# Kernel tuning notes

Hardware: AMD Instinct MI355X
Metric: run time of the kernel (lower is better)

Reference implementation:

```python
import jax, jax.numpy as jnp
import numpy as np

EPS = 1e-5

def _bn(x, g, b):
    # training-mode BatchNorm1d: per-feature batch stats (biased var), affine
    mu = jnp.mean(x, 0)
    var = jnp.var(x, 0)
    return (x - mu) * jax.lax.rsqrt(var + EPS) * g + b

def _sage(x_src, x_dst, src, dst, Wl, bl, Wr):
    # PyG SAGEConv(mean): lin_l(mean_{j in N(i)} x_j) + lin_r(x_i); lin_r has no bias
    n = x_dst.shape[0]
    s = jax.ops.segment_sum(x_src[src], dst, num_segments=n)          # [N_dst, H]
    c = jax.ops.segment_sum(jnp.ones(src.shape, x_src.dtype), dst, num_segments=n)
    m = s / jnp.maximum(c, 1.0)[:, None]                              # mean aggregation; isolated nodes -> 0
    return m @ Wl + bl + x_dst @ Wr


def setup_inputs() -> dict:
    ND, NG, NS = 30000, 60000, 15000
    FD, FG, FS = 256, 128, 64
    H, O = 128, 64
    E = dict(dg=500000, gd=500000, gs=400000, sg=400000, ds=150000, sd=150000)
    keys = iter(jax.random.split(jax.random.key(0), 64))
    def nrm(shape, s=0.05):
        return jax.random.normal(next(keys), shape, jnp.float32) * s
    def ridx(n, hi):
        return jax.random.randint(next(keys), (n,), 0, hi, jnp.int32)
    inp = {
        'x_drug': nrm((ND, FD), 1.0), 'x_gene': nrm((NG, FG), 1.0), 'x_dis': nrm((NS, FS), 1.0),
        'src_dg': ridx(E['dg'], ND), 'dst_dg': ridx(E['dg'], NG),
        'src_gd': ridx(E['gd'], NG), 'dst_gd': ridx(E['gd'], ND),
        'src_gs': ridx(E['gs'], NG), 'dst_gs': ridx(E['gs'], NS),
        'src_sg': ridx(E['sg'], NS), 'dst_sg': ridx(E['sg'], NG),
        'src_ds': ridx(E['ds'], ND), 'dst_ds': ridx(E['ds'], NS),
        'src_sd': ridx(E['sd'], NS), 'dst_sd': ridx(E['sd'], ND),
        # input projections per node type
        'W_in_drug': nrm((FD, H)), 'b_in_drug': jnp.zeros((H,), jnp.float32),
        'W_in_gene': nrm((FG, H)), 'b_in_gene': jnp.zeros((H,), jnp.float32),
        'W_in_dis':  nrm((FS, H)), 'b_in_dis':  jnp.zeros((H,), jnp.float32),
        # input norms, [3 node types, H]
        'g_in': jnp.ones((3, H), jnp.float32), 'bt_in': jnp.zeros((3, H), jnp.float32),
        # SAGEConv weights: [3 layers, 6 edge types, H, H]; order: dg,gd,gs,sg,ds,sd
        'Wl': nrm((3, 6, H, H)), 'Wr': nrm((3, 6, H, H)), 'bl': jnp.zeros((3, 6, H), jnp.float32),
        # per-layer per-type norms [3 layers, 3 types, H]
        'g_conv': jnp.ones((3, 3, H), jnp.float32), 'bt_conv': jnp.zeros((3, 3, H), jnp.float32),
        'W_fin': nrm((H, O)), 'b_fin': jnp.zeros((O,), jnp.float32),
    }
    return inp


def reference(x_drug, x_gene, x_dis,
              src_dg, dst_dg, src_gd, dst_gd, src_gs, dst_gs,
              src_sg, dst_sg, src_ds, dst_ds, src_sd, dst_sd,
              W_in_drug, b_in_drug, W_in_gene, b_in_gene, W_in_dis, b_in_dis,
              g_in, bt_in, Wl, Wr, bl, g_conv, bt_conv, W_fin, b_fin):
    relu = jax.nn.relu
    # input proj + BN + ReLU (dropout in eval mode = identity)
    hd = relu(_bn(x_drug @ W_in_drug + b_in_drug, g_in[0], bt_in[0]))
    hg = relu(_bn(x_gene @ W_in_gene + b_in_gene, g_in[1], bt_in[1]))
    hs = relu(_bn(x_dis  @ W_in_dis  + b_in_dis,  g_in[2], bt_in[2]))
    for L in range(3):
        rd, rg, rs = hd, hg, hs
        # HeteroConv aggr='mean' over the two edge types hitting each dst type
        od = ( _sage(rg, rd, src_gd, dst_gd, Wl[L,1], bl[L,1], Wr[L,1])
             + _sage(rs, rd, src_sd, dst_sd, Wl[L,5], bl[L,5], Wr[L,5]) ) * 0.5
        og = ( _sage(rd, rg, src_dg, dst_dg, Wl[L,0], bl[L,0], Wr[L,0])
             + _sage(rs, rg, src_sg, dst_sg, Wl[L,3], bl[L,3], Wr[L,3]) ) * 0.5
        os_ = ( _sage(rg, rs, src_gs, dst_gs, Wl[L,2], bl[L,2], Wr[L,2])
              + _sage(rd, rs, src_ds, dst_ds, Wl[L,4], bl[L,4], Wr[L,4]) ) * 0.5
        hd = relu(_bn(od,  g_conv[L,0], bt_conv[L,0])) + rd
        hg = relu(_bn(og,  g_conv[L,1], bt_conv[L,1])) + rg
        hs = relu(_bn(os_, g_conv[L,2], bt_conv[L,2])) + rs
    return (hd @ W_fin + b_fin, hg @ W_fin + b_fin, hs @ W_fin + b_fin)
```

## Files before the change

### kernel.cpp

```cpp
#include <hip/hip_runtime.h>
#include <cstddef>
#include <cstdint>

typedef _Float16 f16;
typedef _Float16 f16x8 __attribute__((ext_vector_type(8)));
typedef float f32x4 __attribute__((ext_vector_type(4)));

constexpr int ND = 30000, NG = 60000, NS = 15000;
constexpr float BN_EPS = 1e-5f;
constexpr int NBUCK = 64;
constexpr int TBUCK = 6 * NBUCK;
constexpr int PCHUNK = 4096;

static inline int cdiv(int a, int b){ return (a + b - 1) / b; }


struct BDesc {
    const int* src[6]; const int* dst[6];
    int Ebase[7]; int shift[6]; int N[6];
    int* bCnt; int* bBase; int* bCursor;
    uint2* packed;
    int* offs[6]; int* csr[6];
};

__global__ __launch_bounds__(256) void bhist_k(BDesc bd){
    __shared__ int hist[TBUCK];
    int tid = threadIdx.x;
    for (int i = tid; i < TBUCK; i += 256) hist[i] = 0;
    __syncthreads();
    int Etot = bd.Ebase[6];
    #pragma unroll
    for (int u = 0; u < 16; u++){
        int e = blockIdx.x * PCHUNK + u * 256 + tid;
        if (e < Etot){
            int t = 0;
            #pragma unroll
            for (int i = 1; i < 6; i++) if (e >= bd.Ebase[i]) t = i;
            int d = bd.dst[t][e - bd.Ebase[t]];
            atomicAdd(&hist[t * NBUCK + (d >> bd.shift[t])], 1);
        }
    }
    __syncthreads();
    for (int i = tid; i < TBUCK; i += 256)
        if (hist[i]) atomicAdd(&bd.bCnt[i], hist[i]);
}

__global__ __launch_bounds__(512) void bscan_k(BDesc bd){
    __shared__ int sh[TBUCK];
    int tid = threadIdx.x;
    int my = (tid < TBUCK) ? bd.bCnt[tid] : 0;
    if (tid < TBUCK) sh[tid] = my;
    __syncthreads();
    for (int d = 1; d < TBUCK; d <<= 1){
        int v = (tid < TBUCK) ? sh[tid] : 0;
        int add = (tid >= d && tid < TBUCK) ? sh[tid - d] : 0;
        __syncthreads();
        if (tid < TBUCK) sh[tid] = v + add;
        __syncthreads();
    }
    if (tid < TBUCK){
        int excl = sh[tid] - my;
        bd.bBase[tid] = excl;
        bd.bCursor[tid] = excl;
    }
    if (tid == 0) bd.bBase[TBUCK] = sh[TBUCK - 1];
}

__global__ __launch_bounds__(256) void bpart_k(BDesc bd){
    __shared__ int hist[TBUCK];
    __shared__ int basesh[TBUCK];
    int tid = threadIdx.x;
    for (int i = tid; i < TBUCK; i += 256) hist[i] = 0;
    __syncthreads();
    int Etot = bd.Ebase[6];
    int mb[16], mr[16], ms[16], md[16];
    #pragma unroll
    for (int u = 0; u < 16; u++){
        int e = blockIdx.x * PCHUNK + u * 256 + tid;
        mb[u] = -1;
        if (e < Etot){
            int t = 0;
            #pragma unroll
            for (int i = 1; i < 6; i++) if (e >= bd.Ebase[i]) t = i;
            int le = e - bd.Ebase[t];
            int s = bd.src[t][le], d = bd.dst[t][le];
            int b = t * NBUCK + (d >> bd.shift[t]);
            mr[u] = atomicAdd(&hist[b], 1);
            mb[u] = b; ms[u] = s; md[u] = d;
        }
    }
    __syncthreads();
    for (int i = tid; i < TBUCK; i += 256)
        basesh[i] = hist[i] ? atomicAdd(&bd.bCursor[i], hist[i]) : 0;
    __syncthreads();
    #pragma unroll
    for (int u = 0; u < 16; u++){
        if (mb[u] >= 0){
            int pos = basesh[mb[u]] + mr[u];
            bd.packed[pos] = make_uint2((unsigned)ms[u], (unsigned)md[u]);
        }
    }
}

__global__ __launch_bounds__(256) void bucketCsr_k(BDesc bd){
    __shared__ int cnt[1024];
    __shared__ int sh[256];
    int b = blockIdx.x;
    int t = b >> 6;
    int bb = b & 63;
    int tid = threadIdx.x;
    int shift = bd.shift[t];
    int nodeBase = bb << shift;
    int Nt = bd.N[t];
    int span = 1 << shift;
    int tbase = bd.bBase[t * NBUCK];
    int eBeg = bd.bBase[b], eEnd = bd.bBase[b + 1];
    int bLocal = eBeg - tbase;
    #pragma unroll
    for (int i = 0; i < 4; i++) cnt[tid + i * 256] = 0;
    __syncthreads();
    for (int e = eBeg + tid; e < eEnd; e += 256)
        atomicAdd(&cnt[(int)bd.packed[e].y - nodeBase], 1);
    __syncthreads();
    int c0 = cnt[tid * 4], c1 = cnt[tid * 4 + 1], c2 = cnt[tid * 4 + 2], c3 = cnt[tid * 4 + 3];
    int s = c0 + c1 + c2 + c3;
    sh[tid] = s;
    __syncthreads();
    for (int d = 1; d < 256; d <<= 1){
        int v = sh[tid];
        int add = (tid >= d) ? sh[tid - d] : 0;
        __syncthreads();
        sh[tid] = v + add;
        __syncthreads();
    }
    int run = sh[tid] - s;
    int idx = tid * 4;
    int ex0 = run, ex1 = run + c0, ex2 = ex1 + c1, ex3 = ex2 + c2;
    if (idx     < span && nodeBase + idx     < Nt) bd.offs[t][nodeBase + idx]     = bLocal + ex0;
    if (idx + 1 < span && nodeBase + idx + 1 < Nt) bd.offs[t][nodeBase + idx + 1] = bLocal + ex1;
    if (idx + 2 < span && nodeBase + idx + 2 < Nt) bd.offs[t][nodeBase + idx + 2] = bLocal + ex2;
    if (idx + 3 < span && nodeBase + idx + 3 < Nt) bd.offs[t][nodeBase + idx + 3] = bLocal + ex3;
    cnt[idx] = ex0; cnt[idx + 1] = ex1; cnt[idx + 2] = ex2; cnt[idx + 3] = ex3;
    __syncthreads();
    for (int e = eBeg + tid; e < eEnd; e += 256){
        uint2 p = bd.packed[e];
        int lpos = atomicAdd(&cnt[(int)p.y - nodeBase], 1);
        bd.csr[t][bLocal + lpos] = (int)p.x;
    }
    if (bb == NBUCK - 1 && tid == 0)
        bd.offs[t][Nt] = bd.bBase[(t + 1) * NBUCK] - tbase;
}


struct CastDesc { const float* src[3]; f16* dst[3]; int base[4]; };

__global__ __launch_bounds__(256) void castAll_k(CastDesc cdsc){
    int idx = blockIdx.x * 256 + threadIdx.x;
    if (idx >= cdsc.base[3]) return;
    int t = 0;
    #pragma unroll
    for (int i = 1; i < 3; i++) if (idx >= cdsc.base[i]) t = i;
    int i4 = (idx - cdsc.base[t]) * 4;
    float4 v = *reinterpret_cast<const float4*>(cdsc.src[t] + i4);
    union { uint2 u; f16 h[4]; } o;
    o.h[0] = (f16)v.x; o.h[1] = (f16)v.y; o.h[2] = (f16)v.z; o.h[3] = (f16)v.w;
    *reinterpret_cast<uint2*>(cdsc.dst[t] + i4) = o.u;
}

struct WDesc {
    const float* W_in0; const float* W_in1; const float* W_in2;
    const float* W_fin; const float* Wl; const float* Wr;
    f16* Wint0; f16* Wint1; f16* Wint2; f16* Wfin_t; f16* Wcat_t;
};

__global__ __launch_bounds__(256) void weightAll_k(WDesc wd){
    int idx = blockIdx.x * 256 + threadIdx.x;
    if (idx < 32768){
        int c = idx >> 8, k = idx & 255;
        wd.Wint0[idx] = (f16)wd.W_in0[k * 128 + c];
    } else if (idx < 49152){
        int l = idx - 32768; int c = l >> 7, k = l & 127;
        wd.Wint1[l] = (f16)wd.W_in1[k * 128 + c];
    } else if (idx < 57344){
        int l = idx - 49152; int c = l >> 6, k = l & 63;
        wd.Wint2[l] = (f16)wd.W_in2[k * 128 + c];
    } else if (idx < 65536){
        int l = idx - 57344; int c = l >> 7, k = l & 127;
        wd.Wfin_t[l] = (f16)wd.W_fin[k * 64 + c];
    } else if (idx < 507904){
        int l = idx - 65536;
        int g = l / (384 * 128);
        int rem = l - g * (384 * 128);
        int c = rem / 384;
        int k = rem - c * 384;
        int L = g / 3, t = g - L * 3;
        const int e1s[3] = {1, 0, 2}, e2s[3] = {5, 3, 4};
        int e1 = e1s[t], e2 = e2s[t];
        float v;
        if (k < 128)      v = wd.Wl[(((size_t)L * 6 + e1) * 128 + k) * 128 + c];
        else if (k < 256) v = wd.Wl[(((size_t)L * 6 + e2) * 128 + (k - 128)) * 128 + c];
        else {
            int kr = k - 256;
            v = wd.Wr[(((size_t)L * 6 + e1) * 128 + kr) * 128 + c]
              + wd.Wr[(((size_t)L * 6 + e2) * 128 + kr) * 128 + c];
        }
        wd.Wcat_t[l] = (f16)v;
    }
}


struct GSeg { const int* offs; const int* csr; const uint4* h; uint4* A; int colPair4; int N; int base; };
struct GDesc { GSeg s[6]; const uint4* zrow; };

__device__ __forceinline__ f16x8 as_h8(uint4 v){
    union { uint4 u; f16x8 h; } c; c.u = v; return c.h;
}

__device__ __forceinline__ f16x8 shfl_xor8(f16x8 v, int mask){
    union { f16x8 h; int u[4]; } c; c.h = v;
    #pragma unroll
    for (int i = 0; i < 4; i++) c.u[i] = __shfl_xor(c.u[i], mask);
    return c.h;
}

__global__ __launch_bounds__(256) void gatherall_k(GDesc gd){
    int bid = blockIdx.x;
    int si = 0;
    #pragma unroll
    for (int t = 1; t < 6; t++) if (bid >= gd.s[t].base) si = t;
    GSeg sg = gd.s[si];
    int node = (bid - sg.base) * 4 + (threadIdx.x >> 6);
    if (node >= sg.N) return;
    int lane = threadIdx.x & 63;
    int grp = lane >> 4, li = lane & 15;
    int s = sg.offs[node], e = sg.offs[node + 1];
    const int* cp = sg.csr;
    const uint4* hp = sg.h;
    f16x8 a = {};
    for (int c = s; c < e; c += 64){
        int nchunk = e - c; if (nchunk > 64) nchunk = 64;
        int idx = (lane < nchunk) ? cp[c + lane] : 0;
        int r = 0;
        for (; r + 32 <= nchunk; r += 32){
            int i0 = __shfl(idx, r + grp);
            int i1 = __shfl(idx, r + 4  + grp);
            int i2 = __shfl(idx, r + 8  + grp);
            int i3 = __shfl(idx, r + 12 + grp);
            int i4 = __shfl(idx, r + 16 + grp);
            int i5 = __shfl(idx, r + 20 + grp);
            int i6 = __shfl(idx, r + 24 + grp);
            int i7 = __shfl(idx, r + 28 + grp);
            uint4 v0 = hp[(size_t)i0 * 16 + li];
            uint4 v1 = hp[(size_t)i1 * 16 + li];
            uint4 v2 = hp[(size_t)i2 * 16 + li];
            uint4 v3 = hp[(size_t)i3 * 16 + li];
            uint4 v4 = hp[(size_t)i4 * 16 + li];
            uint4 v5 = hp[(size_t)i5 * 16 + li];
            uint4 v6 = hp[(size_t)i6 * 16 + li];
            uint4 v7 = hp[(size_t)i7 * 16 + li];
            a = a + as_h8(v0); a = a + as_h8(v1); a = a + as_h8(v2); a = a + as_h8(v3);
            a = a + as_h8(v4); a = a + as_h8(v5); a = a + as_h8(v6); a = a + as_h8(v7);
        }
        if (r + 16 <= nchunk){
            int i0 = __shfl(idx, r + grp);
            int i1 = __shfl(idx, r + 4  + grp);
            int i2 = __shfl(idx, r + 8  + grp);
            int i3 = __shfl(idx, r + 12 + grp);
            uint4 v0 = hp[(size_t)i0 * 16 + li];
            uint4 v1 = hp[(size_t)i1 * 16 + li];
            uint4 v2 = hp[(size_t)i2 * 16 + li];
            uint4 v3 = hp[(size_t)i3 * 16 + li];
            a = a + as_h8(v0); a = a + as_h8(v1); a = a + as_h8(v2); a = a + as_h8(v3);
            r += 16;
        }
        for (; r < nchunk; r += 4){
            int ei = __shfl(idx, r + grp);
            const uint4* rp = ((r + grp) < nchunk) ? (hp + (size_t)ei * 16) : gd.zrow;
            a = a + as_h8(rp[li]);
        }
    }
    a = a + shfl_xor8(a, 16);
    a = a + shfl_xor8(a, 32);
    if (grp == 0){
        float inv = (e > s) ? 1.0f / (float)(e - s) : 0.f;
        union { uint4 u; f16 h[8]; } pk;
        #pragma unroll
        for (int i = 0; i < 8; i++) pk.h[i] = (f16)((float)a[i] * inv);
        sg.A[(size_t)node * 32 + sg.colPair4 + li] = pk.u;
    }
}


struct GemmSeg {
    const f16* A1; const f16* A2; const f16* Wt;
    const float* b1; const float* b2; void* out; float* stats;
    int lda1, lda2, ksplit, N, K, tileBase; float scale;
};
struct GemmDesc { GemmSeg s[3]; };

template<int BN, bool STATS, bool OUT16>
__global__ __launch_bounds__(256) void gemmAll_k(GemmDesc gd){
    constexpr int CF = BN / 16;
    __shared__ f16 As[128 * 64];
    __shared__ f16 Bs[BN * 64];
    __shared__ float ssum[BN];
    __shared__ float ssq[BN];
    int bid = blockIdx.x;
    int si = 0;
    #pragma unroll
    for (int t = 1; t < 3; t++) if (bid >= gd.s[t].tileBase) si = t;
    GemmSeg sg = gd.s[si];
    int tid = threadIdx.x;
    int wv = tid >> 6, lane = tid & 63;
    int row0 = (bid - sg.tileBase) * 128;
    int N = sg.N, K = sg.K;
    if (STATS && tid < BN){ ssum[tid] = 0.f; ssq[tid] = 0.f; }

    int rsub = lane >> 3;
    int seg  = lane & 7;
    int sseg = seg ^ rsub;

    f32x4 acc[2][CF];
    #pragma unroll
    for (int rf = 0; rf < 2; rf++)
        #pragma unroll
        for (int cf = 0; cf < CF; cf++)
            acc[rf][cf] = (f32x4){0.f, 0.f, 0.f, 0.f};

    for (int k0 = 0; k0 < K; k0 += 64){
        const f16* Ab; int lda, kloc;
        if (k0 < sg.ksplit){ Ab = sg.A1; lda = sg.lda1; kloc = k0; }
        else               { Ab = sg.A2; lda = sg.lda2; kloc = k0 - sg.ksplit; }
        #pragma unroll
        for (int p = 0; p < 4; p++){
            int r = wv * 32 + p * 8 + rsub;
            const f16* srca = Ab + (size_t)(row0 + r) * lda + kloc + sseg * 8;
            __builtin_amdgcn_global_load_lds(
                (const __attribute__((address_space(1))) void*)srca,
                (__attribute__((address_space(3))) void*)&As[(wv * 32 + p * 8) * 64],
                16, 0, 0);
        }
        #pragma unroll
        for (int p = 0; p < BN / 32; p++){
            int c0 = wv * (BN / 4) + p * 8;
            const f16* srcb = sg.Wt + (size_t)(c0 + rsub) * K + k0 + sseg * 8;
            __builtin_amdgcn_global_load_lds(
                (const __attribute__((address_space(1))) void*)srcb,
                (__attribute__((address_space(3))) void*)&Bs[c0 * 64],
                16, 0, 0);
        }
        __syncthreads();
        #pragma unroll
        for (int kf = 0; kf < 2; kf++){
            int kidx = kf * 4 + (lane >> 4);
            int ar0 = wv * 32 + (lane & 15);
            int ar1 = ar0 + 16;
            f16x8 a0 = *reinterpret_cast<const f16x8*>(&As[ar0 * 64 + ((kidx ^ (ar0 & 7)) * 8)]);
            f16x8 a1 = *reinterpret_cast<const f16x8*>(&As[ar1 * 64 + ((kidx ^ (ar1 & 7)) * 8)]);
            #pragma unroll
            for (int cf = 0; cf < CF; cf++){
                int bc = cf * 16 + (lane & 15);
                f16x8 b = *reinterpret_cast<const f16x8*>(&Bs[bc * 64 + ((kidx ^ (bc & 7)) * 8)]);
                acc[0][cf] = __builtin_amdgcn_mfma_f32_16x16x32_f16(a0, b, acc[0][cf], 0, 0, 0);
                acc[1][cf] = __builtin_amdgcn_mfma_f32_16x16x32_f16(a1, b, acc[1][cf], 0, 0, 0);
            }
        }
        __syncthreads();
    }
    int rbase = row0 + wv * 32 + ((lane >> 4) << 2);
    #pragma unroll
    for (int cf = 0; cf < CF; cf++){
        int col = cf * 16 + (lane & 15);
        float bias = 0.f;
        if (sg.b1) bias += sg.b1[col];
        if (sg.b2) bias += sg.b2[col];
        float ls = 0.f, lq = 0.f;
        #pragma unroll
        for (int rf = 0; rf < 2; rf++){
            #pragma unroll
            for (int q = 0; q < 4; q++){
                int gr = rbase + rf * 16 + q;
                if (gr < N){
                    float v = sg.scale * (acc[rf][cf][q] + bias);
                    if (OUT16) ((f16*)sg.out)[(size_t)gr * BN + col] = (f16)v;
                    else       ((float*)sg.out)[(size_t)gr * BN + col] = v;
                    ls += v; lq += v * v;
                }
            }
        }
        if (STATS){ atomicAdd(&ssum[col], ls); atomicAdd(&ssq[col], lq); }
    }
    if (STATS){
        __syncthreads();
        if (tid < BN){
            atomicAdd(&sg.stats[tid], ssum[tid]);
            atomicAdd(&sg.stats[128 + tid], ssq[tid]);
        }
    }
}


struct BnSeg { const f16* o; const float* stats; const float* g; const float* b; f16* h; int N; float invN; int residual; int idxBase; };
struct BnDesc { BnSeg s[3]; int total; };

__global__ __launch_bounds__(256) void bnAll_k(BnDesc bd){
    int idx = blockIdx.x * 256 + threadIdx.x;
    if (idx >= bd.total) return;
    int si = 0;
    #pragma unroll
    for (int t = 1; t < 3; t++) if (idx >= bd.s[t].idxBase) si = t;
    BnSeg sg = bd.s[si];
    int l = idx - sg.idxBase;
    int n = l >> 4, c8 = (l & 15) * 8;
    union { uint4 u; f16 h[8]; } ov;
    ov.u = *reinterpret_cast<const uint4*>(sg.o + (size_t)n * 128 + c8);
    float r[8];
    #pragma unroll
    for (int j = 0; j < 8; j++){
        int c = c8 + j;
        float mu  = sg.stats[c] * sg.invN;
        float var = sg.stats[128 + c] * sg.invN - mu * mu;
        float v = ((float)ov.h[j] - mu) * rsqrtf(var + BN_EPS) * sg.g[c] + sg.b[c];
        r[j] = v > 0.f ? v : 0.f;
    }
    f16* hp = sg.h + (size_t)n * 128 + c8;
    if (sg.residual){
        uint4 old = *reinterpret_cast<const uint4*>(hp);
        union { uint4 u; f16 h[8]; } ou; ou.u = old;
        #pragma unroll
        for (int j = 0; j < 8; j++) r[j] += (float)ou.h[j];
    }
    union { uint4 u; f16 h[8]; } pk;
    #pragma unroll
    for (int j = 0; j < 8; j++) pk.h[j] = (f16)r[j];
    *reinterpret_cast<uint4*>(hp) = pk.u;
}


extern "C" void kernel_launch(void* const* d_in, const int* in_sizes, int n_in,
                              void* d_out, int out_size, void* d_ws, size_t ws_size,
                              hipStream_t stream){
    const float* x_drug = (const float*)d_in[0];
    const float* x_gene = (const float*)d_in[1];
    const float* x_dis  = (const float*)d_in[2];
    const int* srcP[6] = {(const int*)d_in[3], (const int*)d_in[5], (const int*)d_in[7],
                          (const int*)d_in[9], (const int*)d_in[11], (const int*)d_in[13]};
    const int* dstP[6] = {(const int*)d_in[4], (const int*)d_in[6], (const int*)d_in[8],
                          (const int*)d_in[10], (const int*)d_in[12], (const int*)d_in[14]};
    const int  Et[6]   = {in_sizes[3], in_sizes[5], in_sizes[7], in_sizes[9], in_sizes[11], in_sizes[13]};
    const float* W_in[3] = {(const float*)d_in[15], (const float*)d_in[17], (const float*)d_in[19]};
    const float* b_in[3] = {(const float*)d_in[16], (const float*)d_in[18], (const float*)d_in[20]};
    const float* g_in  = (const float*)d_in[21];
    const float* bt_in = (const float*)d_in[22];
    const float* Wl    = (const float*)d_in[23];
    const float* Wr    = (const float*)d_in[24];
    const float* bl    = (const float*)d_in[25];
    const float* g_conv  = (const float*)d_in[26];
    const float* bt_conv = (const float*)d_in[27];
    const float* W_fin = (const float*)d_in[28];
    const float* b_fin = (const float*)d_in[29];
    float* out = (float*)d_out;

    const int Ndst_t[6]     = {NG, ND, NS, NG, NS, ND};
    const int srcT[6]       = {0, 1, 1, 2, 0, 2};
    const int dstT[6]       = {1, 0, 2, 1, 2, 0};
    const int colPair4_t[6] = {0, 0, 0, 16, 16, 16};

    const int Nn[3]  = {ND, NG, NS};
    const int Kin[3] = {256, 128, 64};
    const float* xin[3] = {x_drug, x_gene, x_dis};

    char* base = (char*)d_ws;
    size_t off = 0;
    auto alloc = [&](size_t bytes) -> char* {
        char* p = base + off; off += (bytes + 255) & ~(size_t)255; return p;
    };
    f16* h[3];  for (int t = 0; t < 3; t++) h[t]  = (f16*)alloc((size_t)Nn[t] * 128 * 2);
    f16* A[3];  for (int t = 0; t < 3; t++) A[t]  = (f16*)alloc((size_t)Nn[t] * 256 * 2);
    f16* xb[3]; for (int t = 0; t < 3; t++) xb[t] = (f16*)alloc((size_t)Nn[t] * Kin[t] * 2);
    f16* Wint[3]; for (int t = 0; t < 3; t++) Wint[t] = (f16*)alloc((size_t)128 * Kin[t] * 2);
    f16* Wfin_t = (f16*)alloc((size_t)64 * 128 * 2);
    f16* Wcat_t = (f16*)alloc((size_t)9 * 128 * 384 * 2);
    char* oPool = alloc((size_t)(ND + NG + NS) * 128 * 2);
    f16* o[3];
    o[0] = (f16*)oPool; o[1] = o[0] + (size_t)ND * 128; o[2] = o[1] + (size_t)NG * 128;
    uint2* packed = (uint2*)oPool;
    float* stats = (float*)alloc(12 * 256 * 4);
    int* zeroPool = (int*)alloc((size_t)(TBUCK + 64) * 4);
    int* bCnt = zeroPool;
    const uint4* zrow = (const uint4*)(zeroPool + TBUCK);
    int* bBase   = (int*)alloc((TBUCK + 1) * 4);
    int* bCursor = (int*)alloc(TBUCK * 4);
    int *offs[6], *csr[6];
    for (int t = 0; t < 6; t++) offs[t] = (int*)alloc((size_t)(Ndst_t[t] + 1) * 4);
    for (int t = 0; t < 6; t++) csr[t]  = (int*)alloc((size_t)Et[t] * 4);

    hipMemsetAsync(zeroPool, 0, (size_t)(TBUCK + 64) * 4, stream);
    hipMemsetAsync(stats, 0, 12 * 256 * 4, stream);

    BDesc bd;
    {
        int ecum = 0;
        for (int t = 0; t < 6; t++){
            bd.src[t] = srcP[t]; bd.dst[t] = dstP[t];
            bd.Ebase[t] = ecum; ecum += Et[t];
            int sft = 0; while (((Ndst_t[t] - 1) >> sft) >= NBUCK) sft++;
            bd.shift[t] = sft;
            bd.N[t] = Ndst_t[t];
            bd.offs[t] = offs[t]; bd.csr[t] = csr[t];
        }
        bd.Ebase[6] = ecum;
        bd.bCnt = bCnt; bd.bBase = bBase; bd.bCursor = bCursor;
        bd.packed = packed;
    }
    int Etot = bd.Ebase[6];
    bhist_k<<<cdiv(Etot, PCHUNK), 256, 0, stream>>>(bd);
    bscan_k<<<1, 512, 0, stream>>>(bd);
    bpart_k<<<cdiv(Etot, PCHUNK), 256, 0, stream>>>(bd);
    bucketCsr_k<<<TBUCK, 256, 0, stream>>>(bd);

    CastDesc cds;
    {
        int b = 0;
        for (int t = 0; t < 3; t++){
            cds.src[t] = xin[t]; cds.dst[t] = xb[t];
            cds.base[t] = b; b += Nn[t] * Kin[t] / 4;
        }
        cds.base[3] = b;
    }
    castAll_k<<<cdiv(cds.base[3], 256), 256, 0, stream>>>(cds);
    WDesc wd = {W_in[0], W_in[1], W_in[2], W_fin, Wl, Wr,
                Wint[0], Wint[1], Wint[2], Wfin_t, Wcat_t};
    weightAll_k<<<cdiv(507904, 256), 256, 0, stream>>>(wd);

    int tiles[3]; for (int t = 0; t < 3; t++) tiles[t] = cdiv(Nn[t], 128);
    int tileBase[4] = {0, tiles[0], tiles[0] + tiles[1], tiles[0] + tiles[1] + tiles[2]};

    {
        GemmDesc g{};
        for (int t = 0; t < 3; t++){
            g.s[t] = {xb[t], xb[t], Wint[t], b_in[t], nullptr, o[t], stats + t * 256,
                      Kin[t], Kin[t], Kin[t], Nn[t], Kin[t], tileBase[t], 1.0f};
        }
        gemmAll_k<128, true, true><<<tileBase[3], 256, 0, stream>>>(g);
        BnDesc bnd{}; int ib = 0;
        for (int t = 0; t < 3; t++){
            bnd.s[t] = {o[t], stats + t * 256, g_in + t * 128, bt_in + t * 128, h[t],
                        Nn[t], 1.0f / Nn[t], 0, ib};
            ib += Nn[t] * 16;
        }
        bnd.total = ib;
        bnAll_k<<<cdiv(ib, 256), 256, 0, stream>>>(bnd);
    }

    const int e1s[3] = {1, 0, 2}, e2s[3] = {5, 3, 4};
    for (int L = 0; L < 3; L++){
        GDesc gd; int bacc = 0;
        gd.zrow = zrow;
        for (int t = 0; t < 6; t++){
            gd.s[t].offs = offs[t];
            gd.s[t].csr  = csr[t];
            gd.s[t].h    = (const uint4*)h[srcT[t]];
            gd.s[t].A    = (uint4*)A[dstT[t]];
            gd.s[t].colPair4 = colPair4_t[t];
            gd.s[t].N    = Ndst_t[t];
            gd.s[t].base = bacc;
            bacc += cdiv(Ndst_t[t], 4);
        }
        gatherall_k<<<bacc, 256, 0, stream>>>(gd);
        GemmDesc g{};
        for (int t = 0; t < 3; t++){
            int e1 = e1s[t], e2 = e2s[t];
            g.s[t] = {A[t], h[t], Wcat_t + (size_t)(L * 3 + t) * 128 * 384,
                      bl + (size_t)(L * 6 + e1) * 128, bl + (size_t)(L * 6 + e2) * 128,
                      o[t], stats + (size_t)(3 + L * 3 + t) * 256,
                      256, 128, 256, Nn[t], 384, tileBase[t], 0.5f};
        }
        gemmAll_k<128, true, true><<<tileBase[3], 256, 0, stream>>>(g);
        BnDesc bnd{}; int ib = 0;
        for (int t = 0; t < 3; t++){
            bnd.s[t] = {o[t], stats + (size_t)(3 + L * 3 + t) * 256,
                        g_conv + (size_t)(L * 3 + t) * 128, bt_conv + (size_t)(L * 3 + t) * 128,
                        h[t], Nn[t], 1.0f / Nn[t], 1, ib};
            ib += Nn[t] * 16;
        }
        bnd.total = ib;
        bnAll_k<<<cdiv(ib, 256), 256, 0, stream>>>(bnd);
    }

    {
        int Ntot = ND + NG + NS;
        GemmDesc g{};
        g.s[0] = {h[0], h[0], Wfin_t, b_fin, nullptr, out, nullptr,
                  128, 128, 128, Ntot, 128, 0, 1.0f};
        g.s[1] = g.s[0]; g.s[1].tileBase = 0x3FFFFFFF; g.s[1].N = 0;
        g.s[2] = g.s[1];
        gemmAll_k<64, false, false><<<cdiv(Ntot, 128), 256, 0, stream>>>(g);
    }
}
```

Measured before the change: 612.3 us.

## Map one 16-lane group per destination node in the neighbor gather kernel

The gather kernel now gives each destination node a 16-lane group instead of a full 64-lane wavefront, so 16 nodes share a block. Each group walks the node's neighbor list 8 at a time, loading indices directly rather than broadcasting them through shuffles. This removes the cross-lane reduction and the idle lanes on low-degree nodes (average degree about 5 to 30). The trade-off is less memory-level parallelism per node for high-degree nodes, redundant index loads across the 16 lanes, and extra loads from the zero row at the end of each list.

```diff
diff --git a/kernel.cpp b/kernel.cpp
--- a/kernel.cpp
+++ b/kernel.cpp
@@ -216,78 +216,39 @@
     union { uint4 u; f16x8 h; } c; c.u = v; return c.h;
 }
 
-__device__ __forceinline__ f16x8 shfl_xor8(f16x8 v, int mask){
-    union { f16x8 h; int u[4]; } c; c.h = v;
-    #pragma unroll
-    for (int i = 0; i < 4; i++) c.u[i] = __shfl_xor(c.u[i], mask);
-    return c.h;
-}
-
 __global__ __launch_bounds__(256) void gatherall_k(GDesc gd){
     int bid = blockIdx.x;
     int si = 0;
     #pragma unroll
     for (int t = 1; t < 6; t++) if (bid >= gd.s[t].base) si = t;
     GSeg sg = gd.s[si];
-    int node = (bid - sg.base) * 4 + (threadIdx.x >> 6);
+    int node = (bid - sg.base) * 16 + (threadIdx.x >> 4);
     if (node >= sg.N) return;
-    int lane = threadIdx.x & 63;
-    int grp = lane >> 4, li = lane & 15;
+    int li = threadIdx.x & 15;
     int s = sg.offs[node], e = sg.offs[node + 1];
     const int* cp = sg.csr;
     const uint4* hp = sg.h;
+    const uint4* zr = gd.zrow;
     f16x8 a = {};
-    for (int c = s; c < e; c += 64){
-        int nchunk = e - c; if (nchunk > 64) nchunk = 64;
-        int idx = (lane < nchunk) ? cp[c + lane] : 0;
-        int r = 0;
-        for (; r + 32 <= nchunk; r += 32){
-            int i0 = __shfl(idx, r + grp);
-            int i1 = __shfl(idx, r + 4  + grp);
-            int i2 = __shfl(idx, r + 8  + grp);
-            int i3 = __shfl(idx, r + 12 + grp);
-            int i4 = __shfl(idx, r + 16 + grp);
-            int i5 = __shfl(idx, r + 20 + grp);
-            int i6 = __shfl(idx, r + 24 + grp);
-            int i7 = __shfl(idx, r + 28 + grp);
-            uint4 v0 = hp[(size_t)i0 * 16 + li];
-            uint4 v1 = hp[(size_t)i1 * 16 + li];
-            uint4 v2 = hp[(size_t)i2 * 16 + li];
-            uint4 v3 = hp[(size_t)i3 * 16 + li];
-            uint4 v4 = hp[(size_t)i4 * 16 + li];
-            uint4 v5 = hp[(size_t)i5 * 16 + li];
-            uint4 v6 = hp[(size_t)i6 * 16 + li];
-            uint4 v7 = hp[(size_t)i7 * 16 + li];
-            a = a + as_h8(v0); a = a + as_h8(v1); a = a + as_h8(v2); a = a + as_h8(v3);
-            a = a + as_h8(v4); a = a + as_h8(v5); a = a + as_h8(v6); a = a + as_h8(v7);
-        }
-        if (r + 16 <= nchunk){
-            int i0 = __shfl(idx, r + grp);
-            int i1 = __shfl(idx, r + 4  + grp);
-            int i2 = __shfl(idx, r + 8  + grp);
-            int i3 = __shfl(idx, r + 12 + grp);
-            uint4 v0 = hp[(size_t)i0 * 16 + li];
-            uint4 v1 = hp[(size_t)i1 * 16 + li];
-            uint4 v2 = hp[(size_t)i2 * 16 + li];
-            uint4 v3 = hp[(size_t)i3 * 16 + li];
-            a = a + as_h8(v0); a = a + as_h8(v1); a = a + as_h8(v2); a = a + as_h8(v3);
-            r += 16;
-        }
-        for (; r < nchunk; r += 4){
-            int ei = __shfl(idx, r + grp);
-            const uint4* rp = ((r + grp) < nchunk) ? (hp + (size_t)ei * 16) : gd.zrow;
-            a = a + as_h8(rp[li]);
-        }
-    }
-    a = a + shfl_xor8(a, 16);
-    a = a + shfl_xor8(a, 32);
-    if (grp == 0){
-        float inv = (e > s) ? 1.0f / (float)(e - s) : 0.f;
-        union { uint4 u; f16 h[8]; } pk;
-        #pragma unroll
-        for (int i = 0; i < 8; i++) pk.h[i] = (f16)((float)a[i] * inv);
-        sg.A[(size_t)node * 32 + sg.colPair4 + li] = pk.u;
-    }
+    for (int j = s; j < e; j += 8){
+        const uint4* p0 = (j + 0 < e) ? (hp + (size_t)cp[j + 0] * 16) : zr;
+        const uint4* p1 = (j + 1 < e) ? (hp + (size_t)cp[j + 1] * 16) : zr;
+        const uint4* p2 = (j + 2 < e) ? (hp + (size_t)cp[j + 2] * 16) : zr;
+        const uint4* p3 = (j + 3 < e) ? (hp + (size_t)cp[j + 3] * 16) : zr;
+        const uint4* p4 = (j + 4 < e) ? (hp + (size_t)cp[j + 4] * 16) : zr;
+        const uint4* p5 = (j + 5 < e) ? (hp + (size_t)cp[j + 5] * 16) : zr;
+        const uint4* p6 = (j + 6 < e) ? (hp + (size_t)cp[j + 6] * 16) : zr;
+        const uint4* p7 = (j + 7 < e) ? (hp + (size_t)cp[j + 7] * 16) : zr;
+        uint4 v0 = p0[li], v1 = p1[li], v2 = p2[li], v3 = p3[li];
+        uint4 v4 = p4[li], v5 = p5[li], v6 = p6[li], v7 = p7[li];
+        a = a + as_h8(v0); a = a + as_h8(v1); a = a + as_h8(v2); a = a + as_h8(v3);
+        a = a + as_h8(v4); a = a + as_h8(v5); a = a + as_h8(v6); a = a + as_h8(v7);
+    }
+    float inv = (e > s) ? 1.0f / (float)(e - s) : 0.f;
+    union { uint4 u; f16 h[8]; } pk;
+    #pragma unroll
+    for (int i = 0; i < 8; i++) pk.h[i] = (f16)((float)a[i] * inv);
+    sg.A[(size_t)node * 32 + sg.colPair4 + li] = pk.u;
 }
 
 
@@ -565,7 +526,7 @@
             gd.s[t].colPair4 = colPair4_t[t];
             gd.s[t].N    = Ndst_t[t];
             gd.s[t].base = bacc;
-            bacc += cdiv(Ndst_t[t], 4);
+            bacc += cdiv(Ndst_t[t], 16);
         }
         gatherall_k<<<bacc, 256, 0, stream>>>(gd);
         GemmDesc g{};
```

Result: faster. 556.1 us (-9.2%).
